# Kernel optimization log

Hardware: AMD Instinct MI355X
Metric: run time of the kernel (lower is better)

Reference implementation:

```python
import jax, jax.numpy as jnp
import numpy as np

NUM_BUCKETS = 14
SCALE_FACTOR = 3.0
MAX_SHAPE = (800, 1333)  # (H, W)
SIDE = int(np.ceil(NUM_BUCKETS / 2.0))  # 7
B, N = 8, 131072


def setup_inputs() -> dict:
    key = jax.random.key(0)
    k1, k2, k3, k4, kc, ko = jax.random.split(key, 6)
    # valid xyxy proposals inside a ~1333x800 image
    x1 = jax.random.uniform(k1, (B, N)) * 1000.0
    y1 = jax.random.uniform(k2, (B, N)) * 600.0
    w = jax.random.uniform(k3, (B, N)) * 300.0 + 16.0
    h = jax.random.uniform(k4, (B, N)) * 300.0 + 16.0
    proposals = jnp.stack([x1, y1, x1 + w, y1 + h], axis=-1)
    cls_preds = jax.random.normal(kc, (B, N * 4 * SIDE), dtype=jnp.float32)
    offset_preds = jax.random.normal(ko, (B, N * 4 * SIDE), dtype=jnp.float32) * 0.5
    return {"proposals": proposals, "cls_preds": cls_preds, "offset_preds": offset_preds}


def reference(proposals, cls_preds, offset_preds):
    batch = cls_preds.shape[0]
    cls = cls_preds.reshape(batch, -1, SIDE)                 # [B, 4N, S]
    scores = jax.nn.softmax(cls, axis=2)
    score_topk, score_label = jax.lax.top_k(scores, 2)      # [B, 4N, 2]

    # bbox_rescale: scale w/h about the box center
    cx = (proposals[..., 0] + proposals[..., 2]) * 0.5
    cy = (proposals[..., 1] + proposals[..., 3]) * 0.5
    pw = (proposals[..., 2] - proposals[..., 0]) * SCALE_FACTOR
    ph = (proposals[..., 3] - proposals[..., 1]) * SCALE_FACTOR
    px1 = cx - 0.5 * pw
    py1 = cy - 0.5 * ph
    px2 = cx + 0.5 * pw
    py2 = cy + 0.5 * ph
    bucket_w = pw / NUM_BUCKETS
    bucket_h = ph / NUM_BUCKETS

    # rows are interleaved (l, r, t, d) per proposal
    inds_l = score_label[:, 0::4, 0]
    inds_r = score_label[:, 1::4, 0]
    inds_t = score_label[:, 2::4, 0]
    inds_d = score_label[:, 3::4, 0]

    f32 = jnp.float32
    l_buckets = px1 + (0.5 + inds_l.astype(f32)) * bucket_w
    r_buckets = px2 - (0.5 + inds_r.astype(f32)) * bucket_w
    t_buckets = py1 + (0.5 + inds_t.astype(f32)) * bucket_h
    d_buckets = py2 - (0.5 + inds_d.astype(f32)) * bucket_h

    offsets = offset_preds.reshape(batch, -1, 4, SIDE)       # [B, N, 4, S]
    l_off = jnp.take_along_axis(offsets[:, :, 0, :], inds_l[..., None], axis=2)[..., 0]
    r_off = jnp.take_along_axis(offsets[:, :, 1, :], inds_r[..., None], axis=2)[..., 0]
    t_off = jnp.take_along_axis(offsets[:, :, 2, :], inds_t[..., None], axis=2)[..., 0]
    d_off = jnp.take_along_axis(offsets[:, :, 3, :], inds_d[..., None], axis=2)[..., 0]

    x1 = l_buckets - l_off * bucket_w
    x2 = r_buckets - r_off * bucket_w
    y1 = t_buckets - t_off * bucket_h
    y2 = d_buckets - d_off * bucket_h

    H, W = MAX_SHAPE
    x1 = jnp.clip(x1, 0.0, W - 1)
    y1 = jnp.clip(y1, 0.0, H - 1)
    x2 = jnp.clip(x2, 0.0, W - 1)
    y2 = jnp.clip(y2, 0.0, H - 1)
    bboxes = jnp.stack([x1, y1, x2, y2], axis=-1)            # [B, N, 4]

    loc_conf = score_topk[:, :, 0]
    top2_neighbor = jnp.abs((score_label[:, :, 0] - score_label[:, :, 1]).astype(f32)) - 1.0
    loc_conf = loc_conf + score_topk[:, :, 1] * top2_neighbor
    loc_conf = loc_conf.reshape(batch, -1, 4).mean(axis=2)   # [B, N]
    return bboxes, loc_conf
```

## Files before the change

kernel.cpp:

```cpp
#include <hip/hip_runtime.h>
#include <math.h>


#define TILE 256
#define PAD_ROW 29

__global__ __launch_bounds__(256) void bucketing_bbox_tile_kernel(
    const float* __restrict__ proposals,
    const float* __restrict__ cls_preds,
    const float* __restrict__ offset_preds,
    float* __restrict__ out_bboxes,
    float* __restrict__ out_conf)
{
    __shared__ float lds[TILE * PAD_ROW];

    const int t = threadIdx.x;
    const size_t base = (size_t)blockIdx.x * TILE;
    const size_t gid = base + t;

    const float4* clsv = reinterpret_cast<const float4*>(cls_preds) + base * 7;
    const float4* offv = reinterpret_cast<const float4*>(offset_preds) + base * 7;
    float4 creg[7], oreg[7];
#pragma unroll
    for (int k = 0; k < 7; ++k) creg[k] = clsv[t + TILE * k];
#pragma unroll
    for (int k = 0; k < 7; ++k) oreg[k] = offv[t + TILE * k];
    float4 pr = reinterpret_cast<const float4*>(proposals)[gid];

    const int p0 = t / 7;
    const int e0 = t - p0 * 7;

    {
        int p = p0, e = e0;
#pragma unroll
        for (int k = 0; k < 7; ++k) {
            int a = p * PAD_ROW + 4 * e;
            lds[a + 0] = creg[k].x;
            lds[a + 1] = creg[k].y;
            lds[a + 2] = creg[k].z;
            lds[a + 3] = creg[k].w;
            p += 36; e += 4;
            if (e >= 7) { e -= 7; p += 1; }
        }
    }
    __syncthreads();

    float cls[28];
    {
        const int rb = t * PAD_ROW;
#pragma unroll
        for (int j = 0; j < 28; ++j) cls[j] = lds[rb + j];
    }

    int   lab0s[4];
    float conf_sum = 0.0f;
#pragma unroll
    for (int s = 0; s < 4; ++s) {
        float best0 = cls[s * 7 + 0];
        float best1 = -INFINITY;
        int   lab0 = 0, lab1 = 0;
#pragma unroll
        for (int j = 1; j < 7; ++j) {
            float x = cls[s * 7 + j];
            bool gt0 = x > best0;
            bool gt1 = x > best1;
            best1 = gt0 ? best0 : (gt1 ? x : best1);
            lab1  = gt0 ? lab0  : (gt1 ? j : lab1);
            best0 = gt0 ? x : best0;
            lab0  = gt0 ? j : lab0;
        }
        float sum = 0.0f;
#pragma unroll
        for (int j = 0; j < 7; ++j) sum += __expf(cls[s * 7 + j] - best0);
        float inv = 1.0f / sum;
        float p0s = inv;
        float p1s = __expf(best1 - best0) * inv;

        lab0s[s] = lab0;
        float neighbor = fabsf((float)(lab0 - lab1)) - 1.0f;
        conf_sum += p0s + p1s * neighbor;
    }
    __syncthreads();

    {
        int p = p0, e = e0;
#pragma unroll
        for (int k = 0; k < 7; ++k) {
            int a = p * PAD_ROW + 4 * e;
            lds[a + 0] = oreg[k].x;
            lds[a + 1] = oreg[k].y;
            lds[a + 2] = oreg[k].z;
            lds[a + 3] = oreg[k].w;
            p += 36; e += 4;
            if (e >= 7) { e -= 7; p += 1; }
        }
    }
    __syncthreads();

    const int rb = t * PAD_ROW;
    float osel0 = lds[rb + 0  + lab0s[0]];
    float osel1 = lds[rb + 7  + lab0s[1]];
    float osel2 = lds[rb + 14 + lab0s[2]];
    float osel3 = lds[rb + 21 + lab0s[3]];

    float cx = (pr.x + pr.z) * 0.5f;
    float cy = (pr.y + pr.w) * 0.5f;
    float pw = (pr.z - pr.x) * 3.0f;
    float ph = (pr.w - pr.y) * 3.0f;
    float px1 = cx - 0.5f * pw;
    float px2 = cx + 0.5f * pw;
    float py1 = cy - 0.5f * ph;
    float py2 = cy + 0.5f * ph;
    float bw = pw / 14.0f;
    float bh = ph / 14.0f;

    float l_b = px1 + (0.5f + (float)lab0s[0]) * bw;
    float r_b = px2 - (0.5f + (float)lab0s[1]) * bw;
    float t_b = py1 + (0.5f + (float)lab0s[2]) * bh;
    float d_b = py2 - (0.5f + (float)lab0s[3]) * bh;

    float x1 = l_b - osel0 * bw;
    float x2 = r_b - osel1 * bw;
    float y1 = t_b - osel2 * bh;
    float y2 = d_b - osel3 * bh;

    const float Wm = 1332.0f;
    const float Hm = 799.0f;
    x1 = fminf(fmaxf(x1, 0.0f), Wm);
    x2 = fminf(fmaxf(x2, 0.0f), Wm);
    y1 = fminf(fmaxf(y1, 0.0f), Hm);
    y2 = fminf(fmaxf(y2, 0.0f), Hm);

    reinterpret_cast<float4*>(out_bboxes)[gid] = make_float4(x1, y1, x2, y2);
    out_conf[gid] = conf_sum * 0.25f;
}

__global__ __launch_bounds__(256) void bucketing_bbox_tail_kernel(
    const float* __restrict__ proposals,
    const float* __restrict__ cls_preds,
    const float* __restrict__ offset_preds,
    float* __restrict__ out_bboxes,
    float* __restrict__ out_conf,
    int start, int total)
{
    int i = start + blockIdx.x * blockDim.x + threadIdx.x;
    if (i >= total) return;

    float4 pr = reinterpret_cast<const float4*>(proposals)[i];
    float cls[28], offs[28];
    {
        const float4* cp = reinterpret_cast<const float4*>(cls_preds + (size_t)i * 28);
        const float4* op = reinterpret_cast<const float4*>(offset_preds + (size_t)i * 28);
#pragma unroll
        for (int k = 0; k < 7; ++k) reinterpret_cast<float4*>(cls)[k] = cp[k];
#pragma unroll
        for (int k = 0; k < 7; ++k) reinterpret_cast<float4*>(offs)[k] = op[k];
    }
    float cx = (pr.x + pr.z) * 0.5f;
    float cy = (pr.y + pr.w) * 0.5f;
    float pw = (pr.z - pr.x) * 3.0f;
    float ph = (pr.w - pr.y) * 3.0f;
    float px1 = cx - 0.5f * pw, px2 = cx + 0.5f * pw;
    float py1 = cy - 0.5f * ph, py2 = cy + 0.5f * ph;
    float bw = pw / 14.0f, bh = ph / 14.0f;

    int lab0s[4]; float offsel[4]; float conf_sum = 0.0f;
#pragma unroll
    for (int s = 0; s < 4; ++s) {
        float best0 = cls[s * 7], best1 = -INFINITY;
        int lab0 = 0, lab1 = 0;
        float osel = offs[s * 7];
#pragma unroll
        for (int j = 1; j < 7; ++j) {
            float x = cls[s * 7 + j], o = offs[s * 7 + j];
            bool gt0 = x > best0, gt1 = x > best1;
            best1 = gt0 ? best0 : (gt1 ? x : best1);
            lab1  = gt0 ? lab0  : (gt1 ? j : lab1);
            best0 = gt0 ? x : best0;
            lab0  = gt0 ? j : lab0;
            osel  = gt0 ? o : osel;
        }
        float sum = 0.0f;
#pragma unroll
        for (int j = 0; j < 7; ++j) sum += __expf(cls[s * 7 + j] - best0);
        float inv = 1.0f / sum;
        lab0s[s] = lab0; offsel[s] = osel;
        conf_sum += inv + __expf(best1 - best0) * inv * (fabsf((float)(lab0 - lab1)) - 1.0f);
    }
    float x1 = px1 + (0.5f + (float)lab0s[0]) * bw - offsel[0] * bw;
    float x2 = px2 - (0.5f + (float)lab0s[1]) * bw - offsel[1] * bw;
    float y1 = py1 + (0.5f + (float)lab0s[2]) * bh - offsel[2] * bh;
    float y2 = py2 - (0.5f + (float)lab0s[3]) * bh - offsel[3] * bh;
    x1 = fminf(fmaxf(x1, 0.0f), 1332.0f);
    x2 = fminf(fmaxf(x2, 0.0f), 1332.0f);
    y1 = fminf(fmaxf(y1, 0.0f), 799.0f);
    y2 = fminf(fmaxf(y2, 0.0f), 799.0f);
    reinterpret_cast<float4*>(out_bboxes)[i] = make_float4(x1, y1, x2, y2);
    out_conf[i] = conf_sum * 0.25f;
}

extern "C" void kernel_launch(void* const* d_in, const int* in_sizes, int n_in,
                              void* d_out, int out_size, void* d_ws, size_t ws_size,
                              hipStream_t stream) {
    const float* proposals    = (const float*)d_in[0];
    const float* cls_preds    = (const float*)d_in[1];
    const float* offset_preds = (const float*)d_in[2];

    int total = in_sizes[0] / 4;

    float* out_bboxes = (float*)d_out;
    float* out_conf   = (float*)d_out + (size_t)total * 4;

    int full_tiles = total / TILE;
    int rem = total - full_tiles * TILE;

    if (full_tiles > 0) {
        bucketing_bbox_tile_kernel<<<full_tiles, TILE, 0, stream>>>(
            proposals, cls_preds, offset_preds, out_bboxes, out_conf);
    }
    if (rem > 0) {
        int start = full_tiles * TILE;
        bucketing_bbox_tail_kernel<<<(rem + 255) / 256, 256, 0, stream>>>(
            proposals, cls_preds, offset_preds, out_bboxes, out_conf, start, total);
    }
}
```

Measured before the change: 261.0 us.

## Make tile kernel persistent with register double-buffered prefetch and split LDS

Replaces the one-tile-per-block kernel with a persistent grid of at most 1024 blocks. Each block loops over tiles and prefetches the next tile's cls, offset and proposal data into a second register set while it processes the current one. Cls and offsets now go to separate LDS buffers written in one pass, which removes one of the barrier rounds per tile. The cost is doubled register use (about 60 float4s live) and twice the LDS per block, both of which cut occupancy on a purely memory-bound streaming kernel.

```diff
diff --git a/kernel.cpp b/kernel.cpp
--- a/kernel.cpp
+++ b/kernel.cpp
@@ -5,52 +5,57 @@
 #define TILE 256
 #define PAD_ROW 29
 
-__global__ __launch_bounds__(256) void bucketing_bbox_tile_kernel(
-    const float* __restrict__ proposals,
-    const float* __restrict__ cls_preds,
-    const float* __restrict__ offset_preds,
-    float* __restrict__ out_bboxes,
-    float* __restrict__ out_conf)
-{
-    __shared__ float lds[TILE * PAD_ROW];
-
-    const int t = threadIdx.x;
-    const size_t base = (size_t)blockIdx.x * TILE;
-    const size_t gid = base + t;
-
-    const float4* clsv = reinterpret_cast<const float4*>(cls_preds) + base * 7;
-    const float4* offv = reinterpret_cast<const float4*>(offset_preds) + base * 7;
-    float4 creg[7], oreg[7];
-#pragma unroll
-    for (int k = 0; k < 7; ++k) creg[k] = clsv[t + TILE * k];
-#pragma unroll
-    for (int k = 0; k < 7; ++k) oreg[k] = offv[t + TILE * k];
-    float4 pr = reinterpret_cast<const float4*>(proposals)[gid];
-
-    const int p0 = t / 7;
-    const int e0 = t - p0 * 7;
-
+struct TileRegs {
+    float4 c[7];
+    float4 o[7];
+    float4 pr;
+};
+
+__device__ __forceinline__ void load_tile(
+    const float4* __restrict__ clsv,
+    const float4* __restrict__ offv,
+    const float4* __restrict__ prv,
+    int tile, int t, TileRegs& R)
+{
+    const size_t base = (size_t)tile * TILE;
+    const float4* cp = clsv + base * 7;
+    const float4* op = offv + base * 7;
+#pragma unroll
+    for (int k = 0; k < 7; ++k) R.c[k] = cp[t + TILE * k];
+#pragma unroll
+    for (int k = 0; k < 7; ++k) R.o[k] = op[t + TILE * k];
+    R.pr = prv[base + t];
+}
+
+__device__ __forceinline__ void process_tile(
+    float* __restrict__ ldsC, float* __restrict__ ldsO,
+    int tile, int t, int p0, int e0,
+    const TileRegs& R,
+    float* __restrict__ out_bboxes, float* __restrict__ out_conf)
+{
     {
         int p = p0, e = e0;
 #pragma unroll
         for (int k = 0; k < 7; ++k) {
             int a = p * PAD_ROW + 4 * e;
-            lds[a + 0] = creg[k].x;
-            lds[a + 1] = creg[k].y;
-            lds[a + 2] = creg[k].z;
-            lds[a + 3] = creg[k].w;
+            ldsC[a + 0] = R.c[k].x;
+            ldsC[a + 1] = R.c[k].y;
+            ldsC[a + 2] = R.c[k].z;
+            ldsC[a + 3] = R.c[k].w;
+            ldsO[a + 0] = R.o[k].x;
+            ldsO[a + 1] = R.o[k].y;
+            ldsO[a + 2] = R.o[k].z;
+            ldsO[a + 3] = R.o[k].w;
             p += 36; e += 4;
             if (e >= 7) { e -= 7; p += 1; }
         }
     }
     __syncthreads();
 
+    const int rb = t * PAD_ROW;
     float cls[28];
-    {
-        const int rb = t * PAD_ROW;
-#pragma unroll
-        for (int j = 0; j < 28; ++j) cls[j] = lds[rb + j];
-    }
+#pragma unroll
+    for (int j = 0; j < 28; ++j) cls[j] = ldsC[rb + j];
 
     int   lab0s[4];
     float conf_sum = 0.0f;
@@ -73,66 +78,84 @@
 #pragma unroll
         for (int j = 0; j < 7; ++j) sum += __expf(cls[s * 7 + j] - best0);
         float inv = 1.0f / sum;
-        float p0s = inv;
-        float p1s = __expf(best1 - best0) * inv;
-
+        float pA = inv;
+        float pB = __expf(best1 - best0) * inv;
         lab0s[s] = lab0;
-        float neighbor = fabsf((float)(lab0 - lab1)) - 1.0f;
-        conf_sum += p0s + p1s * neighbor;
-    }
-    __syncthreads();
-
-    {
-        int p = p0, e = e0;
-#pragma unroll
-        for (int k = 0; k < 7; ++k) {
-            int a = p * PAD_ROW + 4 * e;
-            lds[a + 0] = oreg[k].x;
-            lds[a + 1] = oreg[k].y;
-            lds[a + 2] = oreg[k].z;
-            lds[a + 3] = oreg[k].w;
-            p += 36; e += 4;
-            if (e >= 7) { e -= 7; p += 1; }
-        }
-    }
-    __syncthreads();
-
-    const int rb = t * PAD_ROW;
-    float osel0 = lds[rb + 0  + lab0s[0]];
-    float osel1 = lds[rb + 7  + lab0s[1]];
-    float osel2 = lds[rb + 14 + lab0s[2]];
-    float osel3 = lds[rb + 21 + lab0s[3]];
-
+        conf_sum += pA + pB * (fabsf((float)(lab0 - lab1)) - 1.0f);
+    }
+
+    float osel0 = ldsO[rb + 0  + lab0s[0]];
+    float osel1 = ldsO[rb + 7  + lab0s[1]];
+    float osel2 = ldsO[rb + 14 + lab0s[2]];
+    float osel3 = ldsO[rb + 21 + lab0s[3]];
+
+    float4 pr = R.pr;
     float cx = (pr.x + pr.z) * 0.5f;
     float cy = (pr.y + pr.w) * 0.5f;
     float pw = (pr.z - pr.x) * 3.0f;
     float ph = (pr.w - pr.y) * 3.0f;
-    float px1 = cx - 0.5f * pw;
-    float px2 = cx + 0.5f * pw;
-    float py1 = cy - 0.5f * ph;
-    float py2 = cy + 0.5f * ph;
-    float bw = pw / 14.0f;
-    float bh = ph / 14.0f;
-
-    float l_b = px1 + (0.5f + (float)lab0s[0]) * bw;
-    float r_b = px2 - (0.5f + (float)lab0s[1]) * bw;
-    float t_b = py1 + (0.5f + (float)lab0s[2]) * bh;
-    float d_b = py2 - (0.5f + (float)lab0s[3]) * bh;
-
-    float x1 = l_b - osel0 * bw;
-    float x2 = r_b - osel1 * bw;
-    float y1 = t_b - osel2 * bh;
-    float y2 = d_b - osel3 * bh;
-
-    const float Wm = 1332.0f;
-    const float Hm = 799.0f;
-    x1 = fminf(fmaxf(x1, 0.0f), Wm);
-    x2 = fminf(fmaxf(x2, 0.0f), Wm);
-    y1 = fminf(fmaxf(y1, 0.0f), Hm);
-    y2 = fminf(fmaxf(y2, 0.0f), Hm);
-
+    float px1 = cx - 0.5f * pw, px2 = cx + 0.5f * pw;
+    float py1 = cy - 0.5f * ph, py2 = cy + 0.5f * ph;
+    float bw = pw / 14.0f, bh = ph / 14.0f;
+
+    float x1 = px1 + (0.5f + (float)lab0s[0]) * bw - osel0 * bw;
+    float x2 = px2 - (0.5f + (float)lab0s[1]) * bw - osel1 * bw;
+    float y1 = py1 + (0.5f + (float)lab0s[2]) * bh - osel2 * bh;
+    float y2 = py2 - (0.5f + (float)lab0s[3]) * bh - osel3 * bh;
+
+    x1 = fminf(fmaxf(x1, 0.0f), 1332.0f);
+    x2 = fminf(fmaxf(x2, 0.0f), 1332.0f);
+    y1 = fminf(fmaxf(y1, 0.0f), 799.0f);
+    y2 = fminf(fmaxf(y2, 0.0f), 799.0f);
+
+    const size_t gid = (size_t)tile * TILE + t;
     reinterpret_cast<float4*>(out_bboxes)[gid] = make_float4(x1, y1, x2, y2);
     out_conf[gid] = conf_sum * 0.25f;
+
+    __syncthreads();
+}
+
+__global__ __launch_bounds__(256) void bucketing_bbox_pipe_kernel(
+    const float* __restrict__ proposals,
+    const float* __restrict__ cls_preds,
+    const float* __restrict__ offset_preds,
+    float* __restrict__ out_bboxes,
+    float* __restrict__ out_conf,
+    int ntiles)
+{
+    __shared__ float ldsC[TILE * PAD_ROW];
+    __shared__ float ldsO[TILE * PAD_ROW];
+
+    const int t = threadIdx.x;
+    int tile = blockIdx.x;
+    if (tile >= ntiles) return;
+
+    const int p0 = t / 7;
+    const int e0 = t - p0 * 7;
+    const int G = gridDim.x;
+
+    const float4* clsv = reinterpret_cast<const float4*>(cls_preds);
+    const float4* offv = reinterpret_cast<const float4*>(offset_preds);
+    const float4* prv  = reinterpret_cast<const float4*>(proposals);
+
+    TileRegs RA, RB;
+    load_tile(clsv, offv, prv, tile, t, RA);
+
+    for (;;) {
+        int tn = tile + G;
+        bool hn = (tn < ntiles);
+        if (hn) load_tile(clsv, offv, prv, tn, t, RB);
+        process_tile(ldsC, ldsO, tile, t, p0, e0, RA, out_bboxes, out_conf);
+        if (!hn) break;
+        tile = tn;
+
+        tn = tile + G;
+        hn = (tn < ntiles);
+        if (hn) load_tile(clsv, offv, prv, tn, t, RA);
+        process_tile(ldsC, ldsO, tile, t, p0, e0, RB, out_bboxes, out_conf);
+        if (!hn) break;
+        tile = tn;
+    }
 }
 
 __global__ __launch_bounds__(256) void bucketing_bbox_tail_kernel(
@@ -211,15 +234,16 @@
     float* out_bboxes = (float*)d_out;
     float* out_conf   = (float*)d_out + (size_t)total * 4;
 
-    int full_tiles = total / TILE;
-    int rem = total - full_tiles * TILE;
-
-    if (full_tiles > 0) {
-        bucketing_bbox_tile_kernel<<<full_tiles, TILE, 0, stream>>>(
-            proposals, cls_preds, offset_preds, out_bboxes, out_conf);
+    int ntiles = total / TILE;
+    int rem = total - ntiles * TILE;
+
+    if (ntiles > 0) {
+        int grid = ntiles < 1024 ? ntiles : 1024;
+        bucketing_bbox_pipe_kernel<<<grid, TILE, 0, stream>>>(
+            proposals, cls_preds, offset_preds, out_bboxes, out_conf, ntiles);
     }
     if (rem > 0) {
-        int start = full_tiles * TILE;
+        int start = ntiles * TILE;
         bucketing_bbox_tail_kernel<<<(rem + 255) / 256, 256, 0, stream>>>(
             proposals, cls_preds, offset_preds, out_bboxes, out_conf, start, total);
     }
```

Result: slower. 268.1 us (+2.7%).
